# Kernel tuning notes

Measured on AMD Instinct MI355X. Metric: run time of the kernel, lower is better.

## Reference

```python
import jax, jax.numpy as jnp
import numpy as np

T, B, S, D = 128, 32, 100, 256  # targetL, batch, sourceL, output_size
EPS = 1e-6

def setup_inputs() -> dict:
    key = jax.random.key(0)
    ks = jax.random.split(key, 9)
    sc = 0.05  # weight init scale
    inp = {
        'prev_layer': jax.random.normal(ks[0], (T, B, D), dtype=jnp.float32),
        'hidden': jax.random.normal(ks[1], (B, D), dtype=jnp.float32),
        'enc_output': jax.random.normal(ks[2], (T * B, S, D), dtype=jnp.float32),
        # linear weights (layer_norm=True -> no biases on linears)
        'W_in': jax.random.normal(ks[3], (D, 3 * D), dtype=jnp.float32) * sc,
        'W_hid': jax.random.normal(ks[4], (D, D), dtype=jnp.float32) * sc,
        'W_ctx': jax.random.normal(ks[5], (D, D), dtype=jnp.float32) * sc,
        'W_enc': jax.random.normal(ks[6], (D, D), dtype=jnp.float32) * sc,
        'W_q': jax.random.normal(ks[7], (D, D), dtype=jnp.float32) * sc,   # MLPAttention query proj
        'v_att': jax.random.normal(ks[8], (D,), dtype=jnp.float32) * sc,  # MLPAttention score vector
        # layernorm affine params
        'g_pre': jnp.ones(3 * D, jnp.float32), 'b_pre': jnp.zeros(3 * D, jnp.float32),
        'g_enc': jnp.ones(D, jnp.float32), 'b_enc': jnp.zeros(D, jnp.float32),
        'g_h': jnp.ones(D, jnp.float32), 'b_h': jnp.zeros(D, jnp.float32),
        'g_c': jnp.ones(D, jnp.float32), 'b_c': jnp.zeros(D, jnp.float32),
        'g_q': jnp.ones(D, jnp.float32), 'b_q': jnp.zeros(D, jnp.float32),
    }
    return inp

def _ln(x, g, b):
    m = jnp.mean(x, axis=-1, keepdims=True)
    v = jnp.mean((x - m) ** 2, axis=-1, keepdims=True)
    return g * (x - m) / jnp.sqrt(v + EPS) + b

def reference(prev_layer, hidden, enc_output, W_in, W_hid, W_ctx, W_enc, W_q, v_att,
              g_pre, b_pre, g_enc, b_enc, g_h, b_h, g_c, b_c, g_q, b_q):
    Tl, Bb, Dd = prev_layer.shape
    # input / encoder projections (dropout=0 -> identity)
    preact = _ln(prev_layer @ W_in, g_pre, b_pre)        # [T,B,3D]
    pctx = _ln(enc_output @ W_enc, g_enc, b_enc)         # [T*B,S,D]
    z, h_gate, x_t = jnp.split(preact, 3, axis=-1)
    z = jax.nn.sigmoid(z)
    h_gate = jax.nn.sigmoid(h_gate)
    # SRU-style elementwise linear recurrence over time
    def step(h, zx):
        zt, xt = zx
        s = (1.0 - zt) * h + zt * xt
        return s, s
    final_h, ss = jax.lax.scan(step, hidden, (z, x_t))   # ss: [T,B,D]
    # MLP (Bahdanau) attention: scores = v . tanh(LN(Wq s) + pctx)
    q = _ln(ss @ W_q, g_q, b_q).reshape(Tl * Bb, 1, Dd)
    scores = jnp.einsum('nsd,d->ns', jnp.tanh(q + pctx), v_att)  # [T*B,S]
    attn = jax.nn.softmax(scores, axis=-1)
    attn_out = jnp.einsum('ns,nsd->nd', attn, pctx).reshape(Tl, Bb, Dd)
    attn_out = attn_out / np.sqrt(Dd).astype(np.float32)
    out = jnp.tanh(_ln(ss @ W_hid, g_h, b_h) + _ln(attn_out @ W_ctx, g_c, b_c))
    out = (1.0 - h_gate) * out + h_gate * prev_layer     # highway gate
    return out, final_h, attn
```

## Files before the change

kernel.cpp:

```cpp
#include <hip/hip_runtime.h>
#include <hip/hip_bf16.h>
#include <math.h>

typedef short  s16x8 __attribute__((ext_vector_type(8)));
typedef float  f32x4 __attribute__((ext_vector_type(4)));
typedef float  f32x2 __attribute__((ext_vector_type(2)));

#define LN_EPS 1e-6f

__device__ __forceinline__ unsigned short f2bf(float x) {
  union { float f; unsigned u; } v; v.f = x;
  unsigned r = v.u + 0x7FFFu + ((v.u >> 16) & 1u);
  return (unsigned short)(r >> 16);
}
__device__ __forceinline__ float bf2f(unsigned short u) {
  union { unsigned u; float f; } v; v.u = ((unsigned)u) << 16;
  return v.f;
}
__device__ __forceinline__ float bflo(unsigned u) {
  union { unsigned u; float f; } v; v.u = u << 16; return v.f;
}
__device__ __forceinline__ float bfhi(unsigned u) {
  union { unsigned u; float f; } v; v.u = u & 0xFFFF0000u; return v.f;
}
__device__ __forceinline__ unsigned pack_bf2(float a, float b) {
  __hip_bfloat162 h = __float22bfloat162_rn(make_float2(a, b));
  unsigned u; __builtin_memcpy(&u, &h, 4); return u;
}
__device__ __forceinline__ float fast_tanh(float x) {
  float e = __expf(2.0f * x);
  return 1.0f - 2.0f * __builtin_amdgcn_rcpf(e + 1.0f);
}
__device__ __forceinline__ float fast_sigmoid(float x) {
  return __builtin_amdgcn_rcpf(1.0f + __expf(-x));
}

template <int CTRL>
__device__ __forceinline__ float dpp_add(float v) {
  union { float f; int i; } a, r;
  a.f = v;
  r.i = __builtin_amdgcn_update_dpp(0, a.i, CTRL, 0xF, 0xF, true);
  return v + r.f;
}
template <int CTRL>
__device__ __forceinline__ float dpp_max(float v) {
  union { float f; int i; } a, r;
  a.f = v;
  r.i = __builtin_amdgcn_update_dpp(a.i, a.i, CTRL, 0xF, 0xF, false);
  return fmaxf(v, r.f);
}
__device__ __forceinline__ float bcast63(float v) {
  union { float f; int i; } a, r;
  a.f = v;
  r.i = __builtin_amdgcn_readlane(a.i, 63);
  return r.f;
}
__device__ __forceinline__ float wredsum(float v) {
  v = dpp_add<0x128>(v); v = dpp_add<0x124>(v); v = dpp_add<0x122>(v); v = dpp_add<0x121>(v);
  v = dpp_add<0x142>(v); v = dpp_add<0x143>(v);
  return bcast63(v);
}
__device__ __forceinline__ float wredmax(float v) {
  v = dpp_max<0x128>(v); v = dpp_max<0x124>(v); v = dpp_max<0x122>(v); v = dpp_max<0x121>(v);
  v = dpp_max<0x142>(v); v = dpp_max<0x143>(v);
  return bcast63(v);
}
__device__ __forceinline__ float red16(float v) {
  v = dpp_add<0x121>(v); v = dpp_add<0x122>(v); v = dpp_add<0x124>(v); v = dpp_add<0x128>(v);
  return v;
}

__device__ __forceinline__ f32x4 mfma16(s16x8 a, s16x8 b, f32x4 c) {
  return __builtin_amdgcn_mfma_f32_16x16x32_bf16(a, b, c, 0, 0, 0);
}

__device__ __forceinline__ void stage_rows(unsigned short* A, const float* src,
                                           int rows, int tid, int nthreads) {
  char* Ab = (char*)A;
  int nquads = rows * 64;
  #pragma unroll 4
  for (int p = tid; p < nquads; p += nthreads) {
    int row = p >> 6, kq = p & 63;
    f32x4 v = *(const f32x4*)(src + row * 256 + kq * 4);
    unsigned u0 = pack_bf2(v.x, v.y);
    unsigned u1 = pack_bf2(v.z, v.w);
    int byte = row * 512 + ((kq * 8) ^ ((row & 7) << 4));
    *(uint2*)(Ab + byte) = uint2{u0, u1};
  }
}

__device__ __forceinline__ s16x8 readA(const unsigned short* A, int row, int kk, int hi) {
  const char* Ab = (const char*)A;
  int byte = row * 512 + (((kk * 64) + hi * 16) ^ ((row & 7) << 4));
  return *(const s16x8*)(Ab + byte);
}
__device__ __forceinline__ s16x8 readB(const unsigned short* Bt, int col, int kk, int hi) {
  return *(const s16x8*)(Bt + col * 256 + kk * 32 + hi * 8);
}

__global__ __launch_bounds__(256) void k_convw(
    const float* Win, const float* Wq, const float* Whid, const float* Wctx, const float* Wenc,
    unsigned short* bt_in, unsigned short* bt_q, unsigned short* bt_hid,
    unsigned short* bt_ctx, unsigned short* bt_enc) {
  __shared__ unsigned short tile[32][34];
  int b = blockIdx.x;
  const float* src; unsigned short* dst; int N, tk, tn; bool perm = false;
  if (b < 192) { src = Win; dst = bt_in; N = 768; tk = b & 7; tn = b >> 3; }
  else {
    int bb = b - 192; int m = bb >> 6; int r = bb & 63;
    tk = r & 7; tn = r >> 3; N = 256;
    src = (m == 0) ? Wq : (m == 1) ? Whid : (m == 2) ? Wctx : Wenc;
    dst = (m == 0) ? bt_q : (m == 1) ? bt_hid : (m == 2) ? bt_ctx : bt_enc;
    perm = (m == 3);
  }
  int k0 = tk * 32, n0 = tn * 32;
  {
    int i = threadIdx.x >> 3, j4 = (threadIdx.x & 7) * 4;
    f32x4 v = *(const f32x4*)(src + (size_t)(k0 + i) * N + n0 + j4);
    *(unsigned*)((char*)&tile[i][j4])     = pack_bf2(v.x, v.y);
    *(unsigned*)((char*)&tile[i][j4 + 2]) = pack_bf2(v.z, v.w);
  }
  __syncthreads();
  {
    int j = threadIdx.x >> 3, i4 = (threadIdx.x & 7) * 4;
    int c = n0 + j;
    int dr = perm ? ((c & ~31) | ((c & 31) >> 1) | ((c & 1) << 4)) : c;
    unsigned lo = (unsigned)tile[i4 + 0][j] | ((unsigned)tile[i4 + 1][j] << 16);
    unsigned hi = (unsigned)tile[i4 + 2][j] | ((unsigned)tile[i4 + 3][j] << 16);
    *(uint2*)(dst + (size_t)dr * 256 + k0 + i4) = uint2{lo, hi};
  }
}

__global__ __launch_bounds__(256) void k_preact(
    const float* prev, const unsigned short* bt_in,
    const float* g_pre, const float* b_pre,
    float* Z, float* HG, float* XT) {
  __shared__ __align__(16) unsigned short A[16 * 256];
  __shared__ float C[16 * 768];
  int tid = threadIdx.x, lane = tid & 63, wave = tid >> 6;
  int hi = lane >> 4, lo = lane & 15;
  int r0 = blockIdx.x * 16;
  stage_rows(A, prev + (size_t)r0 * 256, 16, tid, 256);
  __syncthreads();
  f32x4 acc[12];
  #pragma unroll
  for (int ct = 0; ct < 12; ct++) acc[ct] = f32x4{0.f, 0.f, 0.f, 0.f};
  #pragma unroll
  for (int kk = 0; kk < 8; kk++) {
    s16x8 a = readA(A, lo, kk, hi);
    #pragma unroll
    for (int ct = 0; ct < 12; ct++) {
      s16x8 b = readB(bt_in, wave * 192 + ct * 16 + lo, kk, hi);
      acc[ct] = mfma16(a, b, acc[ct]);
    }
  }
  #pragma unroll
  for (int ct = 0; ct < 12; ct++) {
    int col = wave * 192 + ct * 16 + lo;
    #pragma unroll
    for (int r = 0; r < 4; r++) C[(hi * 4 + r) * 768 + col] = acc[ct][r];
  }
  __syncthreads();
  #pragma unroll
  for (int mm = 0; mm < 4; mm++) {
    int m = wave * 4 + mm;
    float x[12]; float s = 0.f, q = 0.f;
    #pragma unroll
    for (int i = 0; i < 12; i++) {
      x[i] = C[m * 768 + lane + 64 * i];
      s += x[i]; q += x[i] * x[i];
    }
    s = wredsum(s); q = wredsum(q);
    float mean = s * (1.0f / 768.0f);
    float var = q * (1.0f / 768.0f) - mean * mean;
    float rstd = rsqrtf(var + LN_EPS);
    int gr = r0 + m;
    #pragma unroll
    for (int i = 0; i < 12; i++) {
      int c = lane + 64 * i;
      float y = g_pre[c] * (x[i] - mean) * rstd + b_pre[c];
      if (c < 256)      Z [gr * 256 + c]         = fast_sigmoid(y);
      else if (c < 512) HG[gr * 256 + (c - 256)] = fast_sigmoid(y);
      else              XT[gr * 256 + (c - 512)] = y;
    }
  }
}

__global__ __launch_bounds__(256) void k_scan(
    const float* hidden, const float* Z, const float* XT,
    float* SS, float* outFinalH) {
  int tid = blockIdx.x * 256 + threadIdx.x;
  float h = hidden[tid];
  for (int t0 = 0; t0 < 128; t0 += 8) {
    float zc[8], xc[8];
    #pragma unroll
    for (int j = 0; j < 8; j++) {
      zc[j] = Z [(t0 + j) * 8192 + tid];
      xc[j] = XT[(t0 + j) * 8192 + tid];
    }
    #pragma unroll
    for (int j = 0; j < 8; j++) {
      h = (1.0f - zc[j]) * h + zc[j] * xc[j];
      SS[(t0 + j) * 8192 + tid] = h;
    }
  }
  outFinalH[tid] = h;
}

__global__ __launch_bounds__(256) void k_qproj(
    const float* SS, const unsigned short* bt_q,
    const float* g_q, const float* b_q, float* Q) {
  __shared__ __align__(16) unsigned short A[16 * 256];
  __shared__ float C[16 * 256];
  int tid = threadIdx.x, lane = tid & 63, wave = tid >> 6;
  int hi = lane >> 4, lo = lane & 15;
  int r0 = blockIdx.x * 16;
  stage_rows(A, SS + (size_t)r0 * 256, 16, tid, 256);
  __syncthreads();
  f32x4 acc[4];
  #pragma unroll
  for (int ct = 0; ct < 4; ct++) acc[ct] = f32x4{0.f, 0.f, 0.f, 0.f};
  #pragma unroll
  for (int kk = 0; kk < 8; kk++) {
    s16x8 a = readA(A, lo, kk, hi);
    #pragma unroll
    for (int ct = 0; ct < 4; ct++) {
      s16x8 b = readB(bt_q, wave * 64 + ct * 16 + lo, kk, hi);
      acc[ct] = mfma16(a, b, acc[ct]);
    }
  }
  #pragma unroll
  for (int ct = 0; ct < 4; ct++) {
    int col = wave * 64 + ct * 16 + lo;
    #pragma unroll
    for (int r = 0; r < 4; r++) C[(hi * 4 + r) * 256 + col] = acc[ct][r];
  }
  __syncthreads();
  #pragma unroll
  for (int mm = 0; mm < 4; mm++) {
    int m = wave * 4 + mm;
    float x[4]; float s = 0.f, q = 0.f;
    #pragma unroll
    for (int i = 0; i < 4; i++) {
      x[i] = C[m * 256 + lane + 64 * i];
      s += x[i]; q += x[i] * x[i];
    }
    s = wredsum(s); q = wredsum(q);
    float mean = s * (1.0f / 256.0f);
    float var = q * (1.0f / 256.0f) - mean * mean;
    float rstd = rsqrtf(var + LN_EPS);
    int gr = r0 + m;
    #pragma unroll
    for (int i = 0; i < 4; i++) {
      int c = lane + 64 * i;
      Q[gr * 256 + c] = g_q[c] * (x[i] - mean) * rstd + b_q[c];
    }
  }
}

__global__ __launch_bounds__(512, 4) void k_attn(
    const float* enc, const unsigned short* bt_enc, const float* Q,
    const float* g_enc, const float* b_enc, const float* v_att,
    float* AOUT, float* attnOut) {
  __shared__ __align__(16) unsigned short AP[100 * 256];
  __shared__ __align__(16) float alpha[112];
  __shared__ __align__(16) f32x2 stats[112];
  __shared__ float beta_s;
  f32x2* statp = (f32x2*)AP;
  float* spart = (float*)((char*)AP + 16384);
  int n = blockIdx.x;
  int tid = threadIdx.x, lane = tid & 63, wave = tid >> 6;
  int hi = lane >> 4, lo = lane & 15;
  {
    const float* src = enc + (size_t)n * 25600;
    char* Ab = (char*)AP;
    #pragma unroll
    for (int i = 0; i < 12; i++) {
      int p = tid + i * 512;
      int row = p >> 6, kq = p & 63;
      f32x4 v = *(const f32x4*)(src + row * 256 + kq * 4);
      unsigned u0 = pack_bf2(v.x, v.y), u1 = pack_bf2(v.z, v.w);
      int byte = row * 512 + ((kq * 8) ^ ((row & 7) << 4));
      *(uint2*)(Ab + byte) = uint2{u0, u1};
    }
    if (tid < 256) {
      int p = 6144 + tid;
      int row = p >> 6, kq = p & 63;
      f32x4 v = *(const f32x4*)(src + row * 256 + kq * 4);
      unsigned u0 = pack_bf2(v.x, v.y), u1 = pack_bf2(v.z, v.w);
      int byte = row * 512 + ((kq * 8) ^ ((row & 7) << 4));
      *(uint2*)(Ab + byte) = uint2{u0, u1};
    }
  }
  __syncthreads();
  f32x4 acc[7][2];
  #pragma unroll
  for (int mt = 0; mt < 7; mt++) {
    acc[mt][0] = f32x4{0.f, 0.f, 0.f, 0.f};
    acc[mt][1] = f32x4{0.f, 0.f, 0.f, 0.f};
  }
  #pragma unroll
  for (int kk = 0; kk < 8; kk++) {
    s16x8 b0 = readB(bt_enc, wave * 32 + lo, kk, hi);
    s16x8 b1 = readB(bt_enc, wave * 32 + 16 + lo, kk, hi);
    #pragma unroll
    for (int mt = 0; mt < 7; mt++) {
      int ar = mt * 16 + lo;
      ar = ar > 99 ? 99 : ar;
      s16x8 a = readA(AP, ar, kk, hi);
      acc[mt][0] = mfma16(a, b0, acc[mt][0]);
      acc[mt][1] = mfma16(a, b1, acc[mt][1]);
    }
  }
  __syncthreads();
  unsigned pk[7][4];
  #pragma unroll
  for (int mt = 0; mt < 7; mt++) {
    #pragma unroll
    for (int r = 0; r < 4; r++) {
      unsigned u = pack_bf2(acc[mt][0][r], acc[mt][1][r]);
      pk[mt][r] = u;
      float x0 = bflo(u), x1 = bfhi(u);
      float s = red16(x0 + x1);
      float q = red16(fmaf(x0, x0, x1 * x1));
      if (lo == 0) statp[wave * 112 + mt * 16 + hi * 4 + r] = f32x2{s, q};
    }
  }
  __syncthreads();
  if (tid < 112) {
    float S = 0.f, Qs = 0.f;
    #pragma unroll
    for (int w = 0; w < 8; w++) {
      f32x2 t = statp[w * 112 + tid];
      S += t.x; Qs += t.y;
    }
    float mean = S * (1.0f / 256.0f);
    float var = Qs * (1.0f / 256.0f) - mean * mean;
    stats[tid] = f32x2{mean, rsqrtf(var + LN_EPS)};
  }
  __syncthreads();
  int c0 = (wave << 5) + (lo << 1);
  f32x2 gp = *(const f32x2*)(g_enc + c0);
  f32x2 bp = *(const f32x2*)(b_enc + c0);
  f32x2 vp = *(const f32x2*)(v_att + c0);
  f32x2 qp = *(const f32x2*)(Q + (size_t)n * 256 + c0);
  #pragma unroll
  for (int mt = 0; mt < 7; mt++) {
    #pragma unroll
    for (int r = 0; r < 4; r++) {
      int row = mt * 16 + hi * 4 + r;
      f32x2 st = stats[row];
      float x0 = bflo(pk[mt][r]), x1 = bfhi(pk[mt][r]);
      float t = vp.x * fast_tanh(qp.x + fmaf(gp.x, (x0 - st.x) * st.y, bp.x))
              + vp.y * fast_tanh(qp.y + fmaf(gp.y, (x1 - st.x) * st.y, bp.y));
      t = red16(t);
      if (lo == 0) spart[wave * 112 + row] = t;
    }
  }
  __syncthreads();
  if (wave == 0) {
    int row2 = (lane < 36) ? lane + 64 : lane;
    float s1 = 0.f, s2 = 0.f;
    #pragma unroll
    for (int w = 0; w < 8; w++) {
      s1 += spart[w * 112 + lane];
      s2 += spart[w * 112 + row2];
    }
    s2 = (lane < 36) ? s2 : -INFINITY;
    float mx = wredmax(fmaxf(s1, s2));
    float e1 = __expf(s1 - mx);
    float e2 = (lane < 36) ? __expf(s2 - mx) : 0.f;
    float sm = wredsum(e1 + e2);
    float inv = __builtin_amdgcn_rcpf(sm);
    float p1 = e1 * inv, p2 = e2 * inv;
    f32x2 st1 = stats[lane];
    float a1 = p1 * st1.y, bsum = a1 * st1.x;
    float a2 = 0.f;
    if (lane < 36) {
      f32x2 st2 = stats[lane + 64];
      a2 = p2 * st2.y; bsum = fmaf(a2, st2.x, bsum);
    }
    alpha[lane] = a1;
    if (lane < 48) alpha[lane + 64] = a2;
    float bp_ = wredsum(bsum);
    if (lane == 0) beta_s = bp_;
    attnOut[(size_t)n * 100 + lane] = p1;
    if (lane < 36) attnOut[(size_t)n * 100 + lane + 64] = p2;
  }
  __syncthreads();
  float w0 = 0.f, w1 = 0.f;
  #pragma unroll
  for (int mt = 0; mt < 7; mt++) {
    f32x4 al = *(const f32x4*)(alpha + mt * 16 + hi * 4);
    #pragma unroll
    for (int r = 0; r < 4; r++) {
      w0 = fmaf(al[r], bflo(pk[mt][r]), w0);
      w1 = fmaf(al[r], bfhi(pk[mt][r]), w1);
    }
  }
  w0 += __shfl_xor(w0, 16); w0 += __shfl_xor(w0, 32);
  w1 += __shfl_xor(w1, 16); w1 += __shfl_xor(w1, 32);
  if (lane < 16) {
    float y0 = fmaf(gp.x, w0 - beta_s, bp.x) * 0.0625f;
    float y1 = fmaf(gp.y, w1 - beta_s, bp.y) * 0.0625f;
    *(f32x2*)(AOUT + (size_t)n * 256 + c0) = f32x2{y0, y1};
  }
}

__global__ __launch_bounds__(256) void k_out(
    const float* SS, const float* AOUT,
    const unsigned short* bt_hid, const unsigned short* bt_ctx,
    const float* g_h, const float* b_h, const float* g_c, const float* b_c,
    const float* HG, const float* prev, float* out) {
  __shared__ __align__(16) unsigned short A1[16 * 256];
  __shared__ __align__(16) unsigned short A2[16 * 256];
  __shared__ float C1[16 * 256];
  __shared__ float C2[16 * 256];
  int tid = threadIdx.x, lane = tid & 63, wave = tid >> 6;
  int hi = lane >> 4, lo = lane & 15;
  int r0 = blockIdx.x * 16;
  stage_rows(A1, SS + (size_t)r0 * 256, 16, tid, 256);
  stage_rows(A2, AOUT + (size_t)r0 * 256, 16, tid, 256);
  __syncthreads();
  f32x4 acc1[4], acc2[4];
  #pragma unroll
  for (int ct = 0; ct < 4; ct++) {
    acc1[ct] = f32x4{0.f, 0.f, 0.f, 0.f};
    acc2[ct] = f32x4{0.f, 0.f, 0.f, 0.f};
  }
  #pragma unroll
  for (int kk = 0; kk < 8; kk++) {
    s16x8 a1 = readA(A1, lo, kk, hi);
    s16x8 a2 = readA(A2, lo, kk, hi);
    #pragma unroll
    for (int ct = 0; ct < 4; ct++) {
      int col = wave * 64 + ct * 16 + lo;
      s16x8 b1 = readB(bt_hid, col, kk, hi);
      s16x8 b2 = readB(bt_ctx, col, kk, hi);
      acc1[ct] = mfma16(a1, b1, acc1[ct]);
      acc2[ct] = mfma16(a2, b2, acc2[ct]);
    }
  }
  #pragma unroll
  for (int ct = 0; ct < 4; ct++) {
    int col = wave * 64 + ct * 16 + lo;
    #pragma unroll
    for (int r = 0; r < 4; r++) {
      C1[(hi * 4 + r) * 256 + col] = acc1[ct][r];
      C2[(hi * 4 + r) * 256 + col] = acc2[ct][r];
    }
  }
  __syncthreads();
  #pragma unroll
  for (int mm = 0; mm < 4; mm++) {
    int m = wave * 4 + mm;
    float x1[4], x2[4];
    float s1 = 0.f, q1 = 0.f, s2 = 0.f, q2 = 0.f;
    #pragma unroll
    for (int i = 0; i < 4; i++) {
      x1[i] = C1[m * 256 + lane + 64 * i];
      x2[i] = C2[m * 256 + lane + 64 * i];
      s1 += x1[i]; q1 += x1[i] * x1[i];
      s2 += x2[i]; q2 += x2[i] * x2[i];
    }
    s1 = wredsum(s1); q1 = wredsum(q1);
    s2 = wredsum(s2); q2 = wredsum(q2);
    float mean1 = s1 * (1.0f / 256.0f), var1 = q1 * (1.0f / 256.0f) - mean1 * mean1;
    float mean2 = s2 * (1.0f / 256.0f), var2 = q2 * (1.0f / 256.0f) - mean2 * mean2;
    float rstd1 = rsqrtf(var1 + LN_EPS), rstd2 = rsqrtf(var2 + LN_EPS);
    int gr = r0 + m;
    #pragma unroll
    for (int i = 0; i < 4; i++) {
      int c = lane + 64 * i;
      float y1 = g_h[c] * (x1[i] - mean1) * rstd1 + b_h[c];
      float y2 = g_c[c] * (x2[i] - mean2) * rstd2 + b_c[c];
      float y = fast_tanh(y1 + y2);
      float g = HG[gr * 256 + c];
      float pv = prev[gr * 256 + c];
      out[gr * 256 + c] = (1.0f - g) * y + g * pv;
    }
  }
}

extern "C" void kernel_launch(void* const* d_in, const int* in_sizes, int n_in,
                              void* d_out, int out_size, void* d_ws, size_t ws_size,
                              hipStream_t stream) {
  const float* prev   = (const float*)d_in[0];
  const float* hidden = (const float*)d_in[1];
  const float* enc    = (const float*)d_in[2];
  const float* W_in   = (const float*)d_in[3];
  const float* W_hid  = (const float*)d_in[4];
  const float* W_ctx  = (const float*)d_in[5];
  const float* W_enc  = (const float*)d_in[6];
  const float* W_q    = (const float*)d_in[7];
  const float* v_att  = (const float*)d_in[8];
  const float* g_pre  = (const float*)d_in[9];
  const float* b_pre  = (const float*)d_in[10];
  const float* g_enc  = (const float*)d_in[11];
  const float* b_enc  = (const float*)d_in[12];
  const float* g_h    = (const float*)d_in[13];
  const float* b_h    = (const float*)d_in[14];
  const float* g_c    = (const float*)d_in[15];
  const float* b_c    = (const float*)d_in[16];
  const float* g_q    = (const float*)d_in[17];
  const float* b_q    = (const float*)d_in[18];

  char* ws = (char*)d_ws;
  unsigned short* BT_IN  = (unsigned short*)(ws + 0);
  unsigned short* BT_Q   = (unsigned short*)(ws + 393216);
  unsigned short* BT_HID = (unsigned short*)(ws + 524288);
  unsigned short* BT_CTX = (unsigned short*)(ws + 655360);
  unsigned short* BT_ENC = (unsigned short*)(ws + 786432);
  float* Z    = (float*)(ws + 917504);
  float* HG   = (float*)(ws + 5111808);
  float* XT   = (float*)(ws + 9306112);
  float* SS   = (float*)(ws + 13500416);
  float* Q    = (float*)(ws + 17694720);
  float* AOUT = (float*)(ws + 21889024);

  float* out    = (float*)d_out;
  float* finalH = out + 1048576;
  float* attnO  = out + 1056768;

  k_convw <<<448, 256, 0, stream>>>(W_in, W_q, W_hid, W_ctx, W_enc,
                                    BT_IN, BT_Q, BT_HID, BT_CTX, BT_ENC);
  k_preact<<<256, 256, 0, stream>>>(prev, BT_IN, g_pre, b_pre, Z, HG, XT);
  k_scan  <<<32, 256, 0, stream>>>(hidden, Z, XT, SS, finalH);
  k_qproj <<<256, 256, 0, stream>>>(SS, BT_Q, g_q, b_q, Q);
  k_attn  <<<4096, 512, 0, stream>>>(enc, BT_ENC, Q, g_enc, b_enc, v_att, AOUT, attnO);
  k_out   <<<256, 256, 0, stream>>>(SS, AOUT, BT_HID, BT_CTX,
                                    g_h, b_h, g_c, b_c, HG, prev, out);
}
```

Before: 268.0 us.

## Split encoder tile staging into two K halves to overlap loads with MFMA

```diff
diff --git a/kernel.cpp b/kernel.cpp
--- a/kernel.cpp
+++ b/kernel.cpp
@@ -92,6 +92,10 @@
 __device__ __forceinline__ s16x8 readA(const unsigned short* A, int row, int kk, int hi) {
   const char* Ab = (const char*)A;
   int byte = row * 512 + (((kk * 64) + hi * 16) ^ ((row & 7) << 4));
+  return *(const s16x8*)(Ab + byte);
+}
+__device__ __forceinline__ s16x8 readA128(const char* Ab, int row, int kk, int hi) {
+  int byte = row * 256 + (((kk * 64) + hi * 16) ^ ((row & 7) << 4));
   return *(const s16x8*)(Ab + byte);
 }
 __device__ __forceinline__ s16x8 readB(const unsigned short* Bt, int col, int kk, int hi) {
@@ -262,37 +266,46 @@
     const float* enc, const unsigned short* bt_enc, const float* Q,
     const float* g_enc, const float* b_enc, const float* v_att,
     float* AOUT, float* attnOut) {
-  __shared__ __align__(16) unsigned short AP[100 * 256];
+  __shared__ __align__(16) char AP[2 * 100 * 256];
   __shared__ __align__(16) float alpha[112];
   __shared__ __align__(16) f32x2 stats[112];
   __shared__ float beta_s;
   f32x2* statp = (f32x2*)AP;
-  float* spart = (float*)((char*)AP + 16384);
+  float* spart = (float*)(AP + 16384);
   int n = blockIdx.x;
   int tid = threadIdx.x, lane = tid & 63, wave = tid >> 6;
   int hi = lane >> 4, lo = lane & 15;
+  const float* src = enc + (size_t)n * 25600;
   {
-    const float* src = enc + (size_t)n * 25600;
-    char* Ab = (char*)AP;
-    #pragma unroll
-    for (int i = 0; i < 12; i++) {
+    #pragma unroll
+    for (int i = 0; i < 6; i++) {
       int p = tid + i * 512;
-      int row = p >> 6, kq = p & 63;
+      int row = p >> 5, kq = p & 31;
       f32x4 v = *(const f32x4*)(src + row * 256 + kq * 4);
-      unsigned u0 = pack_bf2(v.x, v.y), u1 = pack_bf2(v.z, v.w);
-      int byte = row * 512 + ((kq * 8) ^ ((row & 7) << 4));
-      *(uint2*)(Ab + byte) = uint2{u0, u1};
-    }
-    if (tid < 256) {
-      int p = 6144 + tid;
-      int row = p >> 6, kq = p & 63;
+      int byte = row * 256 + ((kq * 8) ^ ((row & 7) << 4));
+      *(uint2*)(AP + byte) = uint2{pack_bf2(v.x, v.y), pack_bf2(v.z, v.w)};
+    }
+    if (tid < 128) {
+      int p = 3072 + tid;
+      int row = p >> 5, kq = p & 31;
       f32x4 v = *(const f32x4*)(src + row * 256 + kq * 4);
-      unsigned u0 = pack_bf2(v.x, v.y), u1 = pack_bf2(v.z, v.w);
-      int byte = row * 512 + ((kq * 8) ^ ((row & 7) << 4));
-      *(uint2*)(Ab + byte) = uint2{u0, u1};
-    }
-  }
-  __syncthreads();
+      int byte = row * 256 + ((kq * 8) ^ ((row & 7) << 4));
+      *(uint2*)(AP + byte) = uint2{pack_bf2(v.x, v.y), pack_bf2(v.z, v.w)};
+    }
+  }
+  __syncthreads();
+  f32x4 sv[6]; f32x4 svt;
+  #pragma unroll
+  for (int i = 0; i < 6; i++) {
+    int p = tid + i * 512;
+    int row = p >> 5, kq = p & 31;
+    sv[i] = *(const f32x4*)(src + row * 256 + 128 + kq * 4);
+  }
+  if (tid < 128) {
+    int p = 3072 + tid;
+    int row = p >> 5, kq = p & 31;
+    svt = *(const f32x4*)(src + row * 256 + 128 + kq * 4);
+  }
   f32x4 acc[7][2];
   #pragma unroll
   for (int mt = 0; mt < 7; mt++) {
@@ -300,14 +313,43 @@
     acc[mt][1] = f32x4{0.f, 0.f, 0.f, 0.f};
   }
   #pragma unroll
-  for (int kk = 0; kk < 8; kk++) {
+  for (int kk = 0; kk < 4; kk++) {
     s16x8 b0 = readB(bt_enc, wave * 32 + lo, kk, hi);
     s16x8 b1 = readB(bt_enc, wave * 32 + 16 + lo, kk, hi);
     #pragma unroll
     for (int mt = 0; mt < 7; mt++) {
       int ar = mt * 16 + lo;
       ar = ar > 99 ? 99 : ar;
-      s16x8 a = readA(AP, ar, kk, hi);
+      s16x8 a = readA128(AP, ar, kk, hi);
+      acc[mt][0] = mfma16(a, b0, acc[mt][0]);
+      acc[mt][1] = mfma16(a, b1, acc[mt][1]);
+    }
+  }
+  {
+    #pragma unroll
+    for (int i = 0; i < 6; i++) {
+      int p = tid + i * 512;
+      int row = p >> 5, kq = p & 31;
+      int byte = 25600 + row * 256 + ((kq * 8) ^ ((row & 7) << 4));
+      *(uint2*)(AP + byte) = uint2{pack_bf2(sv[i].x, sv[i].y), pack_bf2(sv[i].z, sv[i].w)};
+    }
+    if (tid < 128) {
+      int p = 3072 + tid;
+      int row = p >> 5, kq = p & 31;
+      int byte = 25600 + row * 256 + ((kq * 8) ^ ((row & 7) << 4));
+      *(uint2*)(AP + byte) = uint2{pack_bf2(svt.x, svt.y), pack_bf2(svt.z, svt.w)};
+    }
+  }
+  __syncthreads();
+  #pragma unroll
+  for (int kk = 0; kk < 4; kk++) {
+    s16x8 b0 = readB(bt_enc, wave * 32 + lo, kk + 4, hi);
+    s16x8 b1 = readB(bt_enc, wave * 32 + 16 + lo, kk + 4, hi);
+    #pragma unroll
+    for (int mt = 0; mt < 7; mt++) {
+      int ar = mt * 16 + lo;
+      ar = ar > 99 ? 99 : ar;
+      s16x8 a = readA128(AP + 25600, ar, kk, hi);
       acc[mt][0] = mfma16(a, b0, acc[mt][0]);
       acc[mt][1] = mfma16(a, b1, acc[mt][1]);
     }
```

Result: no change. 271.4 us (+1.3%).

## Use 1024-thread attention blocks, one 16-column tile per wave, fp32 scores

Applied to the files above, without the earlier changes.

```diff
diff --git a/kernel.cpp b/kernel.cpp
--- a/kernel.cpp
+++ b/kernel.cpp
@@ -104,14 +104,13 @@
     unsigned short* bt_ctx, unsigned short* bt_enc) {
   __shared__ unsigned short tile[32][34];
   int b = blockIdx.x;
-  const float* src; unsigned short* dst; int N, tk, tn; bool perm = false;
+  const float* src; unsigned short* dst; int N, tk, tn;
   if (b < 192) { src = Win; dst = bt_in; N = 768; tk = b & 7; tn = b >> 3; }
   else {
     int bb = b - 192; int m = bb >> 6; int r = bb & 63;
     tk = r & 7; tn = r >> 3; N = 256;
     src = (m == 0) ? Wq : (m == 1) ? Whid : (m == 2) ? Wctx : Wenc;
     dst = (m == 0) ? bt_q : (m == 1) ? bt_hid : (m == 2) ? bt_ctx : bt_enc;
-    perm = (m == 3);
   }
   int k0 = tk * 32, n0 = tn * 32;
   {
@@ -123,11 +122,9 @@
   __syncthreads();
   {
     int j = threadIdx.x >> 3, i4 = (threadIdx.x & 7) * 4;
-    int c = n0 + j;
-    int dr = perm ? ((c & ~31) | ((c & 31) >> 1) | ((c & 1) << 4)) : c;
     unsigned lo = (unsigned)tile[i4 + 0][j] | ((unsigned)tile[i4 + 1][j] << 16);
     unsigned hi = (unsigned)tile[i4 + 2][j] | ((unsigned)tile[i4 + 3][j] << 16);
-    *(uint2*)(dst + (size_t)dr * 256 + k0 + i4) = uint2{lo, hi};
+    *(uint2*)(dst + (size_t)(n0 + j) * 256 + k0 + i4) = uint2{lo, hi};
   }
 }
 
@@ -258,115 +255,102 @@
   }
 }
 
-__global__ __launch_bounds__(512, 4) void k_attn(
+__global__ __launch_bounds__(1024, 8) void k_attn(
     const float* enc, const unsigned short* bt_enc, const float* Q,
     const float* g_enc, const float* b_enc, const float* v_att,
     float* AOUT, float* attnOut) {
-  __shared__ __align__(16) unsigned short AP[100 * 256];
+  __shared__ __align__(16) unsigned short AP[112 * 256];
+  __shared__ float statS[448];
+  __shared__ float statQ[448];
+  __shared__ float spart4[448];
   __shared__ __align__(16) float alpha[112];
-  __shared__ __align__(16) f32x2 stats[112];
+  __shared__ __align__(8) f32x2 stats[112];
   __shared__ float beta_s;
-  f32x2* statp = (f32x2*)AP;
-  float* spart = (float*)((char*)AP + 16384);
   int n = blockIdx.x;
   int tid = threadIdx.x, lane = tid & 63, wave = tid >> 6;
   int hi = lane >> 4, lo = lane & 15;
+  if (tid < 448) { statS[tid] = 0.f; statQ[tid] = 0.f; spart4[tid] = 0.f; }
   {
     const float* src = enc + (size_t)n * 25600;
     char* Ab = (char*)AP;
     #pragma unroll
-    for (int i = 0; i < 12; i++) {
-      int p = tid + i * 512;
+    for (int i = 0; i < 6; i++) {
+      int p = tid + i * 1024;
       int row = p >> 6, kq = p & 63;
       f32x4 v = *(const f32x4*)(src + row * 256 + kq * 4);
-      unsigned u0 = pack_bf2(v.x, v.y), u1 = pack_bf2(v.z, v.w);
       int byte = row * 512 + ((kq * 8) ^ ((row & 7) << 4));
-      *(uint2*)(Ab + byte) = uint2{u0, u1};
+      *(uint2*)(Ab + byte) = uint2{pack_bf2(v.x, v.y), pack_bf2(v.z, v.w)};
     }
     if (tid < 256) {
       int p = 6144 + tid;
       int row = p >> 6, kq = p & 63;
       f32x4 v = *(const f32x4*)(src + row * 256 + kq * 4);
-      unsigned u0 = pack_bf2(v.x, v.y), u1 = pack_bf2(v.z, v.w);
       int byte = row * 512 + ((kq * 8) ^ ((row & 7) << 4));
-      *(uint2*)(Ab + byte) = uint2{u0, u1};
-    }
-  }
-  __syncthreads();
-  f32x4 acc[7][2];
+      *(uint2*)(Ab + byte) = uint2{pack_bf2(v.x, v.y), pack_bf2(v.z, v.w)};
+    } else {
+      int t = tid - 256;
+      int row = 100 + (t >> 6), kq = t & 63;
+      int byte = row * 512 + ((kq * 8) ^ ((row & 7) << 4));
+      *(uint2*)(Ab + byte) = uint2{0u, 0u};
+    }
+  }
+  __syncthreads();
+  f32x4 acc[7];
+  #pragma unroll
+  for (int mt = 0; mt < 7; mt++) acc[mt] = f32x4{0.f, 0.f, 0.f, 0.f};
+  #pragma unroll
+  for (int kk = 0; kk < 8; kk++) {
+    s16x8 b = readB(bt_enc, (wave << 4) + lo, kk, hi);
+    #pragma unroll
+    for (int mt = 0; mt < 7; mt++) {
+      s16x8 a = readA(AP, mt * 16 + lo, kk, hi);
+      acc[mt] = mfma16(a, b, acc[mt]);
+    }
+  }
+  int bank = (wave & 3) * 112;
   #pragma unroll
   for (int mt = 0; mt < 7; mt++) {
-    acc[mt][0] = f32x4{0.f, 0.f, 0.f, 0.f};
-    acc[mt][1] = f32x4{0.f, 0.f, 0.f, 0.f};
-  }
-  #pragma unroll
-  for (int kk = 0; kk < 8; kk++) {
-    s16x8 b0 = readB(bt_enc, wave * 32 + lo, kk, hi);
-    s16x8 b1 = readB(bt_enc, wave * 32 + 16 + lo, kk, hi);
-    #pragma unroll
-    for (int mt = 0; mt < 7; mt++) {
-      int ar = mt * 16 + lo;
-      ar = ar > 99 ? 99 : ar;
-      s16x8 a = readA(AP, ar, kk, hi);
-      acc[mt][0] = mfma16(a, b0, acc[mt][0]);
-      acc[mt][1] = mfma16(a, b1, acc[mt][1]);
-    }
-  }
-  __syncthreads();
-  unsigned pk[7][4];
-  #pragma unroll
-  for (int mt = 0; mt < 7; mt++) {
     #pragma unroll
     for (int r = 0; r < 4; r++) {
-      unsigned u = pack_bf2(acc[mt][0][r], acc[mt][1][r]);
-      pk[mt][r] = u;
-      float x0 = bflo(u), x1 = bfhi(u);
-      float s = red16(x0 + x1);
-      float q = red16(fmaf(x0, x0, x1 * x1));
-      if (lo == 0) statp[wave * 112 + mt * 16 + hi * 4 + r] = f32x2{s, q};
+      int row = mt * 16 + hi * 4 + r;
+      float x = acc[mt][r];
+      float s = red16(x);
+      float q = red16(x * x);
+      if (lo == 0 && row < 100) {
+        atomicAdd(&statS[bank + row], s);
+        atomicAdd(&statQ[bank + row], q);
+      }
     }
   }
   __syncthreads();
   if (tid < 112) {
-    float S = 0.f, Qs = 0.f;
-    #pragma unroll
-    for (int w = 0; w < 8; w++) {
-      f32x2 t = statp[w * 112 + tid];
-      S += t.x; Qs += t.y;
-    }
+    float S  = (statS[tid] + statS[112 + tid]) + (statS[224 + tid] + statS[336 + tid]);
+    float Qs = (statQ[tid] + statQ[112 + tid]) + (statQ[224 + tid] + statQ[336 + tid]);
     float mean = S * (1.0f / 256.0f);
     float var = Qs * (1.0f / 256.0f) - mean * mean;
     stats[tid] = f32x2{mean, rsqrtf(var + LN_EPS)};
   }
   __syncthreads();
-  int c0 = (wave << 5) + (lo << 1);
-  f32x2 gp = *(const f32x2*)(g_enc + c0);
-  f32x2 bp = *(const f32x2*)(b_enc + c0);
-  f32x2 vp = *(const f32x2*)(v_att + c0);
-  f32x2 qp = *(const f32x2*)(Q + (size_t)n * 256 + c0);
+  int c = (wave << 4) + lo;
+  float gp = g_enc[c], bp = b_enc[c], vp = v_att[c], qp = Q[(size_t)n * 256 + c];
   #pragma unroll
   for (int mt = 0; mt < 7; mt++) {
     #pragma unroll
     for (int r = 0; r < 4; r++) {
       int row = mt * 16 + hi * 4 + r;
       f32x2 st = stats[row];
-      float x0 = bflo(pk[mt][r]), x1 = bfhi(pk[mt][r]);
-      float t = vp.x * fast_tanh(qp.x + fmaf(gp.x, (x0 - st.x) * st.y, bp.x))
-              + vp.y * fast_tanh(qp.y + fmaf(gp.y, (x1 - st.x) * st.y, bp.y));
+      float t = vp * fast_tanh(qp + fmaf(gp, (acc[mt][r] - st.x) * st.y, bp));
       t = red16(t);
-      if (lo == 0) spart[wave * 112 + row] = t;
+      if (lo == 0 && row < 100) atomicAdd(&spart4[bank + row], t);
     }
   }
   __syncthreads();
   if (wave == 0) {
-    int row2 = (lane < 36) ? lane + 64 : lane;
-    float s1 = 0.f, s2 = 0.f;
-    #pragma unroll
-    for (int w = 0; w < 8; w++) {
-      s1 += spart[w * 112 + lane];
-      s2 += spart[w * 112 + row2];
-    }
-    s2 = (lane < 36) ? s2 : -INFINITY;
+    int l2 = lane + 64;
+    float s1 = (spart4[lane] + spart4[112 + lane]) + (spart4[224 + lane] + spart4[336 + lane]);
+    float s2 = (lane < 36)
+        ? (spart4[l2] + spart4[112 + l2]) + (spart4[224 + l2] + spart4[336 + l2])
+        : -INFINITY;
     float mx = wredmax(fmaxf(s1, s2));
     float e1 = __expf(s1 - mx);
     float e2 = (lane < 36) ? __expf(s2 - mx) : 0.f;
@@ -377,33 +361,28 @@
     float a1 = p1 * st1.y, bsum = a1 * st1.x;
     float a2 = 0.f;
     if (lane < 36) {
-      f32x2 st2 = stats[lane + 64];
+      f32x2 st2 = stats[l2];
       a2 = p2 * st2.y; bsum = fmaf(a2, st2.x, bsum);
     }
     alpha[lane] = a1;
-    if (lane < 48) alpha[lane + 64] = a2;
+    if (lane < 48) alpha[l2] = a2;
     float bp_ = wredsum(bsum);
     if (lane == 0) beta_s = bp_;
     attnOut[(size_t)n * 100 + lane] = p1;
-    if (lane < 36) attnOut[(size_t)n * 100 + lane + 64] = p2;
-  }
-  __syncthreads();
-  float w0 = 0.f, w1 = 0.f;
+    if (lane < 36) attnOut[(size_t)n * 100 + l2] = p2;
+  }
+  __syncthreads();
+  float w = 0.f;
   #pragma unroll
   for (int mt = 0; mt < 7; mt++) {
     f32x4 al = *(const f32x4*)(alpha + mt * 16 + hi * 4);
     #pragma unroll
-    for (int r = 0; r < 4; r++) {
-      w0 = fmaf(al[r], bflo(pk[mt][r]), w0);
-      w1 = fmaf(al[r], bfhi(pk[mt][r]), w1);
-    }
-  }
-  w0 += __shfl_xor(w0, 16); w0 += __shfl_xor(w0, 32);
-  w1 += __shfl_xor(w1, 16); w1 += __shfl_xor(w1, 32);
+    for (int r = 0; r < 4; r++) w = fmaf(al[r], acc[mt][r], w);
+  }
+  w += __shfl_xor(w, 16); w += __shfl_xor(w, 32);
   if (lane < 16) {
-    float y0 = fmaf(gp.x, w0 - beta_s, bp.x) * 0.0625f;
-    float y1 = fmaf(gp.y, w1 - beta_s, bp.y) * 0.0625f;
-    *(f32x2*)(AOUT + (size_t)n * 256 + c0) = f32x2{y0, y1};
+    float y = fmaf(gp, w - beta_s, bp) * 0.0625f;
+    AOUT[(size_t)n * 256 + c] = y;
   }
 }
 
@@ -471,13 +450,13 @@
     int gr = r0 + m;
     #pragma unroll
     for (int i = 0; i < 4; i++) {
-      int c = lane + 64 * i;
-      float y1 = g_h[c] * (x1[i] - mean1) * rstd1 + b_h[c];
-      float y2 = g_c[c] * (x2[i] - mean2) * rstd2 + b_c[c];
+      int cc = lane + 64 * i;
+      float y1 = g_h[cc] * (x1[i] - mean1) * rstd1 + b_h[cc];
+      float y2 = g_c[cc] * (x2[i] - mean2) * rstd2 + b_c[cc];
       float y = fast_tanh(y1 + y2);
-      float g = HG[gr * 256 + c];
-      float pv = prev[gr * 256 + c];
-      out[gr * 256 + c] = (1.0f - g) * y + g * pv;
+      float g = HG[gr * 256 + cc];
+      float pv = prev[gr * 256 + cc];
+      out[gr * 256 + cc] = (1.0f - g) * y + g * pv;
     }
   }
 }
@@ -527,7 +506,7 @@
   k_preact<<<256, 256, 0, stream>>>(prev, BT_IN, g_pre, b_pre, Z, HG, XT);
   k_scan  <<<32, 256, 0, stream>>>(hidden, Z, XT, SS, finalH);
   k_qproj <<<256, 256, 0, stream>>>(SS, BT_Q, g_q, b_q, Q);
-  k_attn  <<<4096, 512, 0, stream>>>(enc, BT_ENC, Q, g_enc, b_enc, v_att, AOUT, attnO);
+  k_attn  <<<4096, 1024, 0, stream>>>(enc, BT_ENC, Q, g_enc, b_enc, v_att, AOUT, attnO);
   k_out   <<<256, 256, 0, stream>>>(SS, AOUT, BT_HID, BT_CTX,
                                     g_h, b_h, g_c, b_c, HG, prev, out);
 }
```

New measurement: 272.7 us. About the same (+1.7%).
